# Kernel tuning notes

Measured on AMD Instinct MI355X. Metric: run time of the kernel, lower is better.

## Reference

```python
import jax, jax.numpy as jnp
import numpy as np

DIM = 2048
HQ = 32
HKV = 8
HEAD_DIM = DIM // HQ          # 64
GROUP = HQ // HKV             # 4 q-heads per kv-head
B, S = 2, 2048


def setup_inputs() -> dict:
    key = jax.random.key(0)
    ks = jax.random.split(key, 12)
    sc_in = 1.0 / np.sqrt(DIM)   # lecun_normal fan-in scaling
    inp = {
        "q": jax.random.normal(ks[0], (B, S, DIM), jnp.float32),
        "k": jax.random.normal(ks[1], (B, S, DIM), jnp.float32),
        "v": jax.random.normal(ks[2], (B, S, DIM), jnp.float32),
        # causal 0/1 mask: module computes scores -= 1/mask + 1, so 0 -> -inf (masked), 1 -> -2 (softmax-invariant shift)
        "mask": jnp.tril(jnp.ones((S, S), jnp.int32)),
        "Wq": jax.random.normal(ks[3], (DIM, HQ * HEAD_DIM), jnp.float32) * sc_in,
        "bq": jnp.zeros((HQ * HEAD_DIM,), jnp.float32),
        "Wk": jax.random.normal(ks[4], (DIM, HKV * HEAD_DIM), jnp.float32) * sc_in,
        "bk": jnp.zeros((HKV * HEAD_DIM,), jnp.float32),
        "Wv": jax.random.normal(ks[5], (DIM, HKV * HEAD_DIM), jnp.float32) * sc_in,
        "bv": jnp.zeros((HKV * HEAD_DIM,), jnp.float32),
        "Wo": jax.random.normal(ks[6], (DIM, DIM), jnp.float32) * (1.0 / np.sqrt(DIM)),
        "bo": jnp.zeros((DIM,), jnp.float32),
    }
    return inp


def reference(q, k, v, mask, Wq, bq, Wk, bk, Wv, bv, Wo, bo):
    b, s, _ = q.shape
    # projections -> per-head layout
    qx = (q @ Wq + bq).reshape(b, s, HKV, GROUP, HEAD_DIM)   # grouped q-heads
    kx = (k @ Wk + bk).reshape(b, s, HKV, HEAD_DIM)
    vx = (v @ Wv + bv).reshape(b, s, HKV, HEAD_DIM)
    # scores[b, h, g, i, j] = q_i . k_j ; same math as repeating kv heads GROUP times
    scores = jnp.einsum('bihgd,bjhd->bhgij', qx, kx) / jnp.sqrt(
        jnp.asarray(HEAD_DIM, qx.dtype))
    # module's masking: scores -= 1/mask + 1  (mask==0 -> -inf, mask==1 -> -2)
    scores = scores - (1.0 / mask.astype(scores.dtype) + 1.0)
    probs = jax.nn.softmax(scores, axis=-1)
    out = jnp.einsum('bhgij,bjhd->bihgd', probs, vx).reshape(b, s, DIM)
    out = out @ Wo + bo
    return out
```

## Files before the change

kernel.cpp:

```cpp
#include <hip/hip_runtime.h>

typedef unsigned short u16;
typedef unsigned int u32;
typedef __attribute__((ext_vector_type(8))) short short8v;
typedef __attribute__((ext_vector_type(4))) float f32x4;

#define DIM 2048
#define HQN 32
#define HKVN 8
#define HD 64
#define BB 2
#define SS 2048
#define MTOT (BB*SS)
#define NKV (HKVN*HD)

__device__ __forceinline__ u16 f2bf(float f){
  u32 u = __float_as_uint(f);
  u += 0x7FFFu + ((u >> 16) & 1u);
  return (u16)(u >> 16);
}

__device__ __forceinline__ u32 cvtpk(float a, float b){
  u32 r; asm("v_cvt_pk_bf16_f32 %0, %1, %2" : "=v"(r) : "v"(a), "v"(b)); return r;
}

__device__ __forceinline__ void gload_lds16(const void* g, void* l){
  __builtin_amdgcn_global_load_lds((const __attribute__((address_space(1))) u32*)g,
                                   (__attribute__((address_space(3))) u32*)l, 16, 0, 0);
}

#define WAITVM_(N) asm volatile("s_waitcnt vmcnt(" #N ")" ::: "memory")
#define WAITVM(N) WAITVM_(N)
#define CFENCE()  asm volatile("" ::: "memory")
#define BARF()    do { CFENCE(); __builtin_amdgcn_s_barrier(); CFENCE(); } while(0)
#define MF(a,b,cc) __builtin_amdgcn_mfma_f32_16x16x32_bf16((a),(b),(cc),0,0,0)

__global__ __launch_bounds__(256) void cast3_kernel(const float4* __restrict__ q,
                                                    const float4* __restrict__ k,
                                                    const float4* __restrict__ v,
                                                    u16* __restrict__ qo,
                                                    u16* __restrict__ ko,
                                                    u16* __restrict__ vo, int n4){
  const int z = blockIdx.y;
  const float4* in = z==0 ? q : (z==1 ? k : v);
  u16* out = z==0 ? qo : (z==1 ? ko : vo);
  int i = blockIdx.x*256 + threadIdx.x;
  if (i < n4){
    float4 f = in[i];
    union { u16 s[4]; unsigned long long u; } r;
    r.s[0]=f2bf(f.x); r.s[1]=f2bf(f.y); r.s[2]=f2bf(f.z); r.s[3]=f2bf(f.w);
    *(unsigned long long*)(out + (size_t)i*4) = r.u;
  }
}

__global__ __launch_bounds__(256) void transpose4_kernel(const float* __restrict__ Wq,
                                                         const float* __restrict__ Wk,
                                                         const float* __restrict__ Wv,
                                                         const float* __restrict__ Wo,
                                                         u16* __restrict__ WqT,
                                                         u16* __restrict__ WkT,
                                                         u16* __restrict__ WvT,
                                                         u16* __restrict__ WoT){
  const int z = blockIdx.z;
  const float* W = z==0?Wq:(z==1?Wk:(z==2?Wv:Wo));
  u16* WT = z==0?WqT:(z==1?WkT:(z==2?WvT:WoT));
  const int N = (z==1||z==2) ? NKV : DIM;
  const int K = DIM;
  int n0 = blockIdx.x*32, k0 = blockIdx.y*32;
  if (n0 >= N) return;
  __shared__ float tile[32][33];
  int tx = threadIdx.x & 31, ty = threadIdx.x >> 5;
  #pragma unroll
  for (int i=0;i<4;i++){
    int kk = ty + i*8;
    tile[kk][tx] = W[(size_t)(k0+kk)*N + n0 + tx];
  }
  __syncthreads();
  #pragma unroll
  for (int i=0;i<4;i++){
    int n = ty + i*8;
    WT[(size_t)(n0+n)*K + k0 + tx] = f2bf(tile[tx][n]);
  }
}

__global__ __launch_bounds__(512, 2) void gemm_qkv_kernel(const u16* __restrict__ Aq,
                                                          const u16* __restrict__ Ak,
                                                          const u16* __restrict__ Av,
                                                          const u16* __restrict__ BT,
                                                          const float* __restrict__ bq,
                                                          const float* __restrict__ bk,
                                                          const float* __restrict__ bv,
                                                          u16* __restrict__ Qp,
                                                          u16* __restrict__ Kp,
                                                          u16* __restrict__ Vp){
  __shared__ __align__(16) u16 lds[65536];
  char* ldsb = (char*)lds;
  const int t = threadIdx.x, lane = t & 63, w = t >> 6;
  const int wm = w >> 2, wn = w & 3, g = lane >> 4, c = lane & 15;
  int bid = blockIdx.x;
  bid = (bid & 7)*24 + (bid >> 3);
  const int mt = bid / 12, nt = bid - mt*12;
  const int m0 = mt*256, n0 = nt*256;
  const int seg = (n0 >= 2560) ? 2 : (n0 >= 2048 ? 1 : 0);
  const u16* A = seg==0 ? Aq : (seg==1 ? Ak : Av);
  const float* bias = seg==0 ? bq : (seg==1 ? bk : bv);
  const int nbase = seg==0 ? 0 : (seg==1 ? 2048 : 2560);

  const int rA = t >> 3;
  const int kc = ((t & 7) ^ (rA & 7)) * 8;
  const u16* gA = A  + (size_t)(m0 + rA)*DIM + kc;
  const u16* gB = BT + (size_t)(n0 + ((rA>>5)<<6) + (rA & 31))*DIM + kc;

  const u32 ko0 = (u32)((g*16) ^ ((c&7)<<4));
  const u32 ko1 = (u32)((64 + g*16) ^ ((c&7)<<4));
  const u32 aoff = wm*8192 + c*128;
  const u32 boff = wn*4096 + c*128;

#define STGA_(PA, KT, ABASE) do{ \
    gload_lds16(gA + (size_t)(KT)*64 + (size_t)((PA)*64)*DIM,       ldsb + (ABASE) + (PA)*16384 + t*16); \
    gload_lds16(gA + (size_t)(KT)*64 + (size_t)((PA)*64+128)*DIM,   ldsb + (ABASE) + (PA)*16384 + 8192 + t*16); }while(0)
#define STGB_(PB, KT, BBASE) do{ \
    gload_lds16(gB + (size_t)(KT)*64 + (size_t)((PB)*32)*DIM,       ldsb + (BBASE) + (PB)*16384 + t*16); \
    gload_lds16(gB + (size_t)(KT)*64 + (size_t)((PB)*32+128)*DIM,   ldsb + (BBASE) + (PB)*16384 + 8192 + t*16); }while(0)
#define LD8(OFF) (*(const short8v*)(ldsb + (OFF)))

  const f32x4 fzero = {0.f,0.f,0.f,0.f};
  f32x4 acc[8][4];
  #pragma unroll
  for (int i=0;i<8;i++)
    #pragma unroll
    for (int j=0;j<4;j++) acc[i][j] = fzero;

#define MM16(FM0, FN0) do{ __builtin_amdgcn_s_setprio(1); \
    _Pragma("unroll") for (int q=0;q<4;q++) \
      _Pragma("unroll") for (int s=0;s<2;s++){ \
        acc[(FM0)+q][(FN0)+s] = MF(a_[q][0], b_[s][0], acc[(FM0)+q][(FN0)+s]); \
        acc[(FM0)+q][(FN0)+s] = MF(a_[q][1], b_[s][1], acc[(FM0)+q][(FN0)+s]); } \
    __builtin_amdgcn_s_setprio(0); }while(0)

#define RD_A(PABASE) do{ _Pragma("unroll") for (int q=0;q<4;q++){ \
    a_[q][0] = LD8((PABASE) + aoff + q*2048 + ko0); \
    a_[q][1] = LD8((PABASE) + aoff + q*2048 + ko1); } }while(0)
#define RD_B(PBBASE) do{ _Pragma("unroll") for (int q=0;q<2;q++){ \
    b_[q][0] = LD8((PBBASE) + boff + q*2048 + ko0); \
    b_[q][1] = LD8((PBBASE) + boff + q*2048 + ko1); } }while(0)

#define QSTEP(TT, CUR, DOSTG, TAIL) do{ \
    const u32 AC = (CUR)*32768,  BC = 65536 + (CUR)*32768; \
    const u32 AN = (CUR^1)*32768, BN = 65536 + (CUR^1)*32768; \
    short8v a_[4][2], b_[2][2]; \
    RD_A(AC); RD_B(BC); \
    if (DOSTG) STGA_(0, (TT)+1, AN); \
    BARF(); \
    MM16(0,0); \
    if (TAIL) { WAITVM(2); } else { WAITVM(4); } \
    BARF(); \
    RD_B(BC + 16384); \
    if (DOSTG) STGB_(0, (TT)+1, BN); \
    BARF(); \
    MM16(0,2); \
    if (TAIL) { WAITVM(0); } else { WAITVM(4); } \
    BARF(); \
    RD_A(AC + 16384); \
    if (DOSTG) STGB_(1, (TT)+1, BN); \
    BARF(); \
    MM16(4,2); \
    BARF(); \
    RD_B(BC); \
    if (DOSTG) STGA_(1, (TT)+1, AN); \
    BARF(); \
    MM16(4,0); \
    if (!TAIL) { WAITVM(4); } \
    BARF(); \
  }while(0)

  STGA_(0, 0, 0); STGB_(0, 0, 65536); STGB_(1, 0, 65536); STGA_(1, 0, 0);
  WAITVM(0);
  BARF();

  #pragma unroll 1
  for (int tt = 0; tt < 30; tt += 2){
    QSTEP(tt,   0, 1, 0);
    QSTEP(tt+1, 1, 1, 0);
  }
  QSTEP(30, 0, 1, 0);
  QSTEP(31, 1, 0, 1);
#undef QSTEP

  WAITVM(0);
  __syncthreads();

  u16* st = lds + w*8192;
  if (seg == 2){
    #pragma unroll
    for (int fm=0; fm<8; fm++){
      #pragma unroll
      for (int fn=0; fn<4; fn++){
        float bvv = bias[n0 - nbase + wn*64 + fn*16 + c];
        int vbase = (fm>>1)*2048 + fn*512 + (g*16 + c)*8 + (fm&1)*4;
        *(u32*)&st[vbase]     = cvtpk(acc[fm][fn][0]+bvv, acc[fm][fn][1]+bvv);
        *(u32*)&st[vbase + 2] = cvtpk(acc[fm][fn][2]+bvv, acc[fm][fn][3]+bvv);
      }
    }
  } else {
    #pragma unroll
    for (int fm=0; fm<8; fm++){
      #pragma unroll
      for (int fn=0; fn<4; fn++){
        float bvv = bias[n0 - nbase + wn*64 + fn*16 + c];
        int sbase = (fm>>1)*2048 + ((fm&1)*2 + (fn>>1))*512 + (c>>2)*128 + (fn&1)*4 + (c&3);
        #pragma unroll
        for (int r=0; r<4; r++)
          st[sbase + (4*g + r)*8] = f2bf(acc[fm][fn][r] + bvv);
      }
    }
  }
  __syncthreads();
  {
    const int bb = m0 >> 11;
    const int st0 = ((m0 & 2047) >> 5) + wm*4;
    u16* dst;
    if (seg == 0)      dst = Qp + (((size_t)bb*HQN  + (n0>>6)        + wn) << 17);
    else if (seg == 1) dst = Kp + (((size_t)bb*HKVN + ((n0-2048)>>6) + wn) << 17);
    else               dst = Vp + (((size_t)bb*HKVN + ((n0-2560)>>6) + wn) << 17);
    dst += (size_t)st0*2048;
    #pragma unroll
    for (int i=0;i<16;i++)
      *(short8v*)(dst + lane*8 + i*512) = *(const short8v*)(st + lane*8 + i*512);
  }
#undef STGA_
#undef STGB_
#undef RD_A
#undef RD_B
#undef MM16
}

__global__ __launch_bounds__(512, 2) void gemm_o_kernel(const u16* __restrict__ A,
                                                        const u16* __restrict__ BT,
                                                        const float* __restrict__ bias,
                                                        float* __restrict__ C){
  __shared__ __align__(16) u16 lds[49152];
  char* ldsb = (char*)lds;
  const int t = threadIdx.x, lane = t & 63, w = t >> 6;
  const int wm = w >> 2, wn = w & 3, g = lane >> 4, c = lane & 15;
  int bid = blockIdx.x;
  bid = (bid & 7)*32 + (bid >> 3);
  const int m0 = (bid >> 4)*256, n0 = (bid & 15)*128;

  const int rA = t >> 3;
  const int kc = ((t & 7) ^ (rA & 7)) * 8;
  const u16* gA = A  + (size_t)(m0 + rA)*DIM + kc;
  const u16* gB = BT + (size_t)(n0 + ((rA>>4)<<5) + (rA & 15))*DIM + kc;

  const u32 ko0 = (u32)((g*16) ^ ((c&7)<<4));
  const u32 ko1 = (u32)((64 + g*16) ^ ((c&7)<<4));
  const u32 aoff = wm*8192 + c*128;
  const u32 boffo = wn*2048 + c*128;

#define STGA_(PA, KT, ABASE) do{ \
    gload_lds16(gA + (size_t)(KT)*64 + (size_t)((PA)*64)*DIM,       ldsb + (ABASE) + (PA)*16384 + t*16); \
    gload_lds16(gA + (size_t)(KT)*64 + (size_t)((PA)*64+128)*DIM,   ldsb + (ABASE) + (PA)*16384 + 8192 + t*16); }while(0)
#define STGB_(PB, KT, BBASE) do{ \
    gload_lds16(gB + (size_t)(KT)*64 + (size_t)((PB)*16)*DIM,       ldsb + (BBASE) + (PB)*8192 + t*16); }while(0)
#define LD8(OFF) (*(const short8v*)(ldsb + (OFF)))

  const f32x4 fzero = {0.f,0.f,0.f,0.f};
  f32x4 acc[8][2];
  #pragma unroll
  for (int i=0;i<8;i++){ acc[i][0] = fzero; acc[i][1] = fzero; }

#define MMO(FM0, FN) do{ __builtin_amdgcn_s_setprio(1); \
    _Pragma("unroll") for (int q=0;q<4;q++){ \
      acc[(FM0)+q][FN] = MF(a_[q][0], b_[0], acc[(FM0)+q][FN]); \
      acc[(FM0)+q][FN] = MF(a_[q][1], b_[1], acc[(FM0)+q][FN]); } \
    __builtin_amdgcn_s_setprio(0); }while(0)

#define RD_A(PABASE) do{ _Pragma("unroll") for (int q=0;q<4;q++){ \
    a_[q][0] = LD8((PABASE) + aoff + q*2048 + ko0); \
    a_[q][1] = LD8((PABASE) + aoff + q*2048 + ko1); } }while(0)
#define RD_B(PBBASE) do{ \
    b_[0] = LD8((PBBASE) + boffo + ko0); \
    b_[1] = LD8((PBBASE) + boffo + ko1); }while(0)

#define OSTEP(TT, CUR, DOSTG, TAIL) do{ \
    const u32 AC = (CUR)*32768,  BC = 65536 + (CUR)*16384; \
    const u32 AN = (CUR^1)*32768, BN = 65536 + (CUR^1)*16384; \
    short8v a_[4][2], b_[2]; \
    RD_A(AC); RD_B(BC); \
    if (DOSTG) STGA_(0, (TT)+1, AN); \
    BARF(); \
    MMO(0,0); \
    if (TAIL) { WAITVM(2); } else { WAITVM(4); } \
    BARF(); \
    RD_B(BC + 8192); \
    if (DOSTG) STGB_(0, (TT)+1, BN); \
    BARF(); \
    MMO(0,1); \
    if (TAIL) { WAITVM(0); } else { WAITVM(3); } \
    BARF(); \
    RD_A(AC + 16384); \
    if (DOSTG) STGB_(1, (TT)+1, BN); \
    BARF(); \
    MMO(4,1); \
    BARF(); \
    RD_B(BC); \
    if (DOSTG) STGA_(1, (TT)+1, AN); \
    BARF(); \
    MMO(4,0); \
    if (!TAIL) { WAITVM(3); } \
    BARF(); \
  }while(0)

  STGA_(0, 0, 0); STGB_(0, 0, 65536); STGB_(1, 0, 65536); STGA_(1, 0, 0);
  WAITVM(0);
  BARF();

  #pragma unroll 1
  for (int tt = 0; tt < 30; tt += 2){
    OSTEP(tt,   0, 1, 0);
    OSTEP(tt+1, 1, 1, 0);
  }
  OSTEP(30, 0, 1, 0);
  OSTEP(31, 1, 0, 1);
#undef OSTEP

  #pragma unroll
  for (int fm=0; fm<8; fm++){
    #pragma unroll
    for (int fn=0; fn<2; fn++){
      int n = n0 + wn*32 + fn*16 + c;
      float bvv = bias[n];
      #pragma unroll
      for (int r=0; r<4; r++){
        int m = m0 + wm*128 + fm*16 + 4*g + r;
        C[(size_t)m*DIM + n] = acc[fm][fn][r] + bvv;
      }
    }
  }
#undef STGA_
#undef STGB_
#undef RD_A
#undef RD_B
#undef MMO
}

__global__ __launch_bounds__(256) void attn_kernel(const u16* __restrict__ Qp,
                                                   const u16* __restrict__ Kp,
                                                   const u16* __restrict__ Vp,
                                                   u16* __restrict__ Aout){
  const int grp = blockIdx.x & 15;
  const int jj  = blockIdx.x >> 4;
  const int b   = grp >> 3;
  const int hkv = grp & 7;
  const int t = threadIdx.x;
  const int lane = t & 63, w = t >> 6;
  const int g = lane >> 4, c = lane & 15;
  const int hq = hkv*4 + w;

  __shared__ __align__(16) u16 Kt[2][2048];
  __shared__ __align__(16) u16 Vt[2][2048];

  const u16* Kb = Kp + (((size_t)b*HKVN + hkv) << 17);
  const u16* Vb = Vp + (((size_t)b*HKVN + hkv) << 17);
  const u16* Qb = Qp + (((size_t)b*HQN + hq) << 17);
  const float SCL = 0.18033688011112042f;
  const f32x4 fzero = {0.f,0.f,0.f,0.f};

  for (int half = 0; half < 2; ++half){
    const int T = half ? jj : (63 - jj);

    short8v qf[2][2];
    {
      const u16* qs = Qb + (size_t)T*2048 + lane*8;
      qf[0][0] = *(const short8v*)(qs);
      qf[0][1] = *(const short8v*)(qs + 512);
      qf[1][0] = *(const short8v*)(qs + 1024);
      qf[1][1] = *(const short8v*)(qs + 1536);
    }
    float l_r[2] = {0.f, 0.f};
    f32x4 o[2][4];
    #pragma unroll
    for (int qi=0; qi<2; qi++)
      #pragma unroll
      for (int f=0; f<4; f++) o[qi][f] = fzero;

    gload_lds16(Kb + t*8, &Kt[0][t*8]);
    gload_lds16(Vb + t*8, &Vt[0][t*8]);
    asm volatile("s_waitcnt vmcnt(0)" ::: "memory");
    __syncthreads();

    int cur = 0;
    for (int kt = 0; kt <= T; ++kt){
      if (kt < T){
        gload_lds16(Kb + (size_t)(kt+1)*2048 + t*8, &Kt[cur^1][t*8]);
        gload_lds16(Vb + (size_t)(kt+1)*2048 + t*8, &Vt[cur^1][t*8]);
      }
      short8v kf0 = *(const short8v*)&Kt[cur][lane*8];
      short8v kf1 = *(const short8v*)&Kt[cur][512 + lane*8];
      short8v kf2 = *(const short8v*)&Kt[cur][1024 + lane*8];
      short8v kf3 = *(const short8v*)&Kt[cur][1536 + lane*8];
      short8v vf0 = *(const short8v*)&Vt[cur][lane*8];
      short8v vf1 = *(const short8v*)&Vt[cur][512 + lane*8];
      short8v vf2 = *(const short8v*)&Vt[cur][1024 + lane*8];
      short8v vf3 = *(const short8v*)&Vt[cur][1536 + lane*8];
      const bool diag = (kt == T);
      #pragma unroll
      for (int qi=0; qi<2; qi++){
        f32x4 s0 = fzero, s1 = fzero;
        __builtin_amdgcn_s_setprio(1);
        s0 = MF(kf0, qf[qi][0], s0);
        s0 = MF(kf1, qf[qi][1], s0);
        s1 = MF(kf2, qf[qi][0], s1);
        s1 = MF(kf3, qf[qi][1], s1);
        __builtin_amdgcn_s_setprio(0);
        float p0[4], p1[4];
        #pragma unroll
        for (int r=0; r<4; r++){
          p0[r] = __builtin_amdgcn_exp2f(s0[r]*SCL);
          p1[r] = __builtin_amdgcn_exp2f(s1[r]*SCL);
        }
        if (diag){
          const int qloc = qi*16 + c;
          #pragma unroll
          for (int r=0; r<4; r++){
            if (4*g + r      > qloc) p0[r] = 0.f;
            if (16 + 4*g + r > qloc) p1[r] = 0.f;
          }
        }
        l_r[qi] += (p0[0]+p0[1]) + (p0[2]+p0[3]) + (p1[0]+p1[1]) + (p1[2]+p1[3]);
        union { u32 u[4]; short8v v; } pu;
        pu.u[0] = cvtpk(p0[0], p0[1]);
        pu.u[1] = cvtpk(p0[2], p0[3]);
        pu.u[2] = cvtpk(p1[0], p1[1]);
        pu.u[3] = cvtpk(p1[2], p1[3]);
        __builtin_amdgcn_s_setprio(1);
        o[qi][0] = MF(pu.v, vf0, o[qi][0]);
        o[qi][1] = MF(pu.v, vf1, o[qi][1]);
        o[qi][2] = MF(pu.v, vf2, o[qi][2]);
        o[qi][3] = MF(pu.v, vf3, o[qi][3]);
        __builtin_amdgcn_s_setprio(0);
      }
      asm volatile("s_waitcnt vmcnt(0)" ::: "memory");
      __syncthreads();
      cur ^= 1;
    }

    #pragma unroll
    for (int qi=0; qi<2; qi++){
      float ls = l_r[qi];
      ls += __shfl_xor(ls, 16);
      ls += __shfl_xor(ls, 32);
      float li = 1.0f / ls;
      float lf[4];
      #pragma unroll
      for (int r=0; r<4; r++) lf[r] = __shfl(li, 4*g + r);
      #pragma unroll
      for (int f=0; f<4; f++){
        #pragma unroll
        for (int r=0; r<4; r++){
          int q = T*32 + qi*16 + 4*g + r;
          Aout[((size_t)b*SS + q)*DIM + hq*HD + f*16 + c] = f2bf(o[qi][f][r]*lf[r]);
        }
      }
    }
  }
}

extern "C" void kernel_launch(void* const* d_in, const int* in_sizes, int n_in,
                              void* d_out, int out_size, void* d_ws, size_t ws_size,
                              hipStream_t stream){
  const float* q  = (const float*)d_in[0];
  const float* k  = (const float*)d_in[1];
  const float* v  = (const float*)d_in[2];
  const float* Wq = (const float*)d_in[4];
  const float* bq = (const float*)d_in[5];
  const float* Wk = (const float*)d_in[6];
  const float* bk = (const float*)d_in[7];
  const float* Wv = (const float*)d_in[8];
  const float* bv = (const float*)d_in[9];
  const float* Wo = (const float*)d_in[10];
  const float* bo = (const float*)d_in[11];
  float* out = (float*)d_out;

  char* ws = (char*)d_ws;
  u16* q_bf = (u16*)ws; ws += (size_t)MTOT*DIM*2;
  u16* k_bf = (u16*)ws; ws += (size_t)MTOT*DIM*2;
  u16* v_bf = (u16*)ws; ws += (size_t)MTOT*DIM*2;
  u16* WqT  = (u16*)ws; ws += (size_t)DIM*DIM*2;
  u16* WkT  = (u16*)ws; ws += (size_t)NKV*DIM*2;
  u16* WvT  = (u16*)ws; ws += (size_t)NKV*DIM*2;
  u16* WoT  = (u16*)ws; ws += (size_t)DIM*DIM*2;
  u16* Qp   = (u16*)ws; ws += (size_t)MTOT*DIM*2;
  u16* Kp   = (u16*)ws; ws += (size_t)MTOT*NKV*2;
  u16* Vp   = (u16*)ws; ws += (size_t)MTOT*NKV*2;
  u16* attn = (u16*)ws; ws += (size_t)MTOT*DIM*2;

  const int n4 = MTOT*DIM/4;
  cast3_kernel<<<dim3(n4/256, 3), 256, 0, stream>>>((const float4*)q, (const float4*)k,
                                                    (const float4*)v, q_bf, k_bf, v_bf, n4);
  transpose4_kernel<<<dim3(DIM/32, DIM/32, 4), 256, 0, stream>>>(Wq, Wk, Wv, Wo,
                                                                 WqT, WkT, WvT, WoT);
  gemm_qkv_kernel<<<192, 512, 0, stream>>>(q_bf, k_bf, v_bf, WqT,
                                           bq, bk, bv, Qp, Kp, Vp);
  attn_kernel<<<512, 256, 0, stream>>>(Qp, Kp, Vp, attn);
  gemm_o_kernel<<<256, 512, 0, stream>>>(attn, WoT, bo, out);
}
```

Measured before the change: 198.8 us.

## Cut barriers in GEMM steps, widen O-GEMM B tile, use 4-slot KV ring

The QKV GEMM step now keeps both B fragment sets in registers, which removes several barriers per K-step and the reload of B. The output GEMM switches to a 64-wide B tile per wave with two MFMA columns, halving the number of phases and barriers. The attention kernel replaces its double-buffered K/V tiles with a 4-slot LDS ring prefetched three tiles ahead, using partial vmcnt waits instead of a full drain each iteration. Both GEMMs drop to one block per CU in their launch bounds, trading occupancy for more registers.

```diff
diff --git a/kernel.cpp b/kernel.cpp
--- a/kernel.cpp
+++ b/kernel.cpp
@@ -31,8 +31,7 @@
 
 #define WAITVM_(N) asm volatile("s_waitcnt vmcnt(" #N ")" ::: "memory")
 #define WAITVM(N) WAITVM_(N)
-#define CFENCE()  asm volatile("" ::: "memory")
-#define BARF()    do { CFENCE(); __builtin_amdgcn_s_barrier(); CFENCE(); } while(0)
+#define BARF()    do { asm volatile("" ::: "memory"); __builtin_amdgcn_s_barrier(); asm volatile("" ::: "memory"); } while(0)
 #define MF(a,b,cc) __builtin_amdgcn_mfma_f32_16x16x32_bf16((a),(b),(cc),0,0,0)
 
 __global__ __launch_bounds__(256) void cast3_kernel(const float4* __restrict__ q,
@@ -83,7 +82,7 @@
   }
 }
 
-__global__ __launch_bounds__(512, 2) void gemm_qkv_kernel(const u16* __restrict__ Aq,
+__global__ __launch_bounds__(512, 1) void gemm_qkv_kernel(const u16* __restrict__ Aq,
                                                           const u16* __restrict__ Ak,
                                                           const u16* __restrict__ Av,
                                                           const u16* __restrict__ BT,
@@ -131,51 +130,50 @@
     #pragma unroll
     for (int j=0;j<4;j++) acc[i][j] = fzero;
 
-#define MM16(FM0, FN0) do{ __builtin_amdgcn_s_setprio(1); \
-    _Pragma("unroll") for (int q=0;q<4;q++) \
-      _Pragma("unroll") for (int s=0;s<2;s++){ \
-        acc[(FM0)+q][(FN0)+s] = MF(a_[q][0], b_[s][0], acc[(FM0)+q][(FN0)+s]); \
-        acc[(FM0)+q][(FN0)+s] = MF(a_[q][1], b_[s][1], acc[(FM0)+q][(FN0)+s]); } \
-    __builtin_amdgcn_s_setprio(0); }while(0)
-
 #define RD_A(PABASE) do{ _Pragma("unroll") for (int q=0;q<4;q++){ \
     a_[q][0] = LD8((PABASE) + aoff + q*2048 + ko0); \
     a_[q][1] = LD8((PABASE) + aoff + q*2048 + ko1); } }while(0)
-#define RD_B(PBBASE) do{ _Pragma("unroll") for (int q=0;q<2;q++){ \
-    b_[q][0] = LD8((PBBASE) + boff + q*2048 + ko0); \
-    b_[q][1] = LD8((PBBASE) + boff + q*2048 + ko1); } }while(0)
+#define RD_B(DST, PBBASE) do{ _Pragma("unroll") for (int s=0;s<2;s++){ \
+    DST[s][0] = LD8((PBBASE) + boff + s*2048 + ko0); \
+    DST[s][1] = LD8((PBBASE) + boff + s*2048 + ko1); } }while(0)
+
+#define MM16(BSRC, FM0, FN0) do{ __builtin_amdgcn_s_setprio(1); \
+    _Pragma("unroll") for (int q=0;q<4;q++) \
+      _Pragma("unroll") for (int s=0;s<2;s++){ \
+        acc[(FM0)+q][(FN0)+s] = MF(a_[q][0], BSRC[s][0], acc[(FM0)+q][(FN0)+s]); \
+        acc[(FM0)+q][(FN0)+s] = MF(a_[q][1], BSRC[s][1], acc[(FM0)+q][(FN0)+s]); } \
+    __builtin_amdgcn_s_setprio(0); }while(0)
 
 #define QSTEP(TT, CUR, DOSTG, TAIL) do{ \
-    const u32 AC = (CUR)*32768,  BC = 65536 + (CUR)*32768; \
-    const u32 AN = (CUR^1)*32768, BN = 65536 + (CUR^1)*32768; \
-    short8v a_[4][2], b_[2][2]; \
-    RD_A(AC); RD_B(BC); \
+    const u32 AC = (CUR)*32768,  BC2 = 65536 + (CUR)*32768; \
+    const u32 AN = (CUR^1)*32768, BN2 = 65536 + (CUR^1)*32768; \
+    short8v a_[4][2], b0_[2][2], b1_[2][2]; \
+     \
+    RD_A(AC); RD_B(b0_, BC2); \
     if (DOSTG) STGA_(0, (TT)+1, AN); \
-    BARF(); \
-    MM16(0,0); \
+    MM16(b0_, 0, 0); \
     if (TAIL) { WAITVM(2); } else { WAITVM(4); } \
     BARF(); \
-    RD_B(BC + 16384); \
-    if (DOSTG) STGB_(0, (TT)+1, BN); \
-    BARF(); \
-    MM16(0,2); \
+     \
+    RD_B(b1_, BC2 + 16384); \
+    if (DOSTG) STGB_(0, (TT)+1, BN2); \
+    MM16(b1_, 0, 2); \
     if (TAIL) { WAITVM(0); } else { WAITVM(4); } \
     BARF(); \
+     \
     RD_A(AC + 16384); \
-    if (DOSTG) STGB_(1, (TT)+1, BN); \
+    if (DOSTG) STGB_(1, (TT)+1, BN2); \
+    MM16(b1_, 4, 2); \
     BARF(); \
-    MM16(4,2); \
-    BARF(); \
-    RD_B(BC); \
+     \
     if (DOSTG) STGA_(1, (TT)+1, AN); \
-    BARF(); \
-    MM16(4,0); \
+    MM16(b0_, 4, 0); \
     if (!TAIL) { WAITVM(4); } \
     BARF(); \
   }while(0)
 
   STGA_(0, 0, 0); STGB_(0, 0, 65536); STGB_(1, 0, 65536); STGA_(1, 0, 0);
-  WAITVM(0);
+  WAITVM(4);
   BARF();
 
   #pragma unroll 1
@@ -235,7 +233,7 @@
 #undef MM16
 }
 
-__global__ __launch_bounds__(512, 2) void gemm_o_kernel(const u16* __restrict__ A,
+__global__ __launch_bounds__(512, 1) void gemm_o_kernel(const u16* __restrict__ A,
                                                         const u16* __restrict__ BT,
                                                         const float* __restrict__ bias,
                                                         float* __restrict__ C){
@@ -250,18 +248,19 @@
   const int rA = t >> 3;
   const int kc = ((t & 7) ^ (rA & 7)) * 8;
   const u16* gA = A  + (size_t)(m0 + rA)*DIM + kc;
-  const u16* gB = BT + (size_t)(n0 + ((rA>>4)<<5) + (rA & 15))*DIM + kc;
+  const u16* gB = BT + (size_t)(n0 + rA)*DIM + kc;
 
   const u32 ko0 = (u32)((g*16) ^ ((c&7)<<4));
   const u32 ko1 = (u32)((64 + g*16) ^ ((c&7)<<4));
   const u32 aoff = wm*8192 + c*128;
-  const u32 boffo = wn*2048 + c*128;
+  const u32 boffo = wn*4096 + c*128;
 
 #define STGA_(PA, KT, ABASE) do{ \
     gload_lds16(gA + (size_t)(KT)*64 + (size_t)((PA)*64)*DIM,       ldsb + (ABASE) + (PA)*16384 + t*16); \
     gload_lds16(gA + (size_t)(KT)*64 + (size_t)((PA)*64+128)*DIM,   ldsb + (ABASE) + (PA)*16384 + 8192 + t*16); }while(0)
-#define STGB_(PB, KT, BBASE) do{ \
-    gload_lds16(gB + (size_t)(KT)*64 + (size_t)((PB)*16)*DIM,       ldsb + (BBASE) + (PB)*8192 + t*16); }while(0)
+#define STGB_O(KT, BBASE) do{ \
+    gload_lds16(gB + (size_t)(KT)*64,                     ldsb + (BBASE) + t*16); \
+    gload_lds16(gB + (size_t)(KT)*64 + (size_t)64*DIM,    ldsb + (BBASE) + 8192 + t*16); }while(0)
 #define LD8(OFF) (*(const short8v*)(ldsb + (OFF)))
 
   const f32x4 fzero = {0.f,0.f,0.f,0.f};
@@ -269,50 +268,40 @@
   #pragma unroll
   for (int i=0;i<8;i++){ acc[i][0] = fzero; acc[i][1] = fzero; }
 
-#define MMO(FM0, FN) do{ __builtin_amdgcn_s_setprio(1); \
-    _Pragma("unroll") for (int q=0;q<4;q++){ \
-      acc[(FM0)+q][FN] = MF(a_[q][0], b_[0], acc[(FM0)+q][FN]); \
-      acc[(FM0)+q][FN] = MF(a_[q][1], b_[1], acc[(FM0)+q][FN]); } \
-    __builtin_amdgcn_s_setprio(0); }while(0)
-
 #define RD_A(PABASE) do{ _Pragma("unroll") for (int q=0;q<4;q++){ \
     a_[q][0] = LD8((PABASE) + aoff + q*2048 + ko0); \
     a_[q][1] = LD8((PABASE) + aoff + q*2048 + ko1); } }while(0)
-#define RD_B(PBBASE) do{ \
-    b_[0] = LD8((PBBASE) + boffo + ko0); \
-    b_[1] = LD8((PBBASE) + boffo + ko1); }while(0)
+#define RD_BO(BBASE) do{ _Pragma("unroll") for (int s=0;s<2;s++){ \
+    b_[s][0] = LD8((BBASE) + boffo + s*2048 + ko0); \
+    b_[s][1] = LD8((BBASE) + boffo + s*2048 + ko1); } }while(0)
+
+#define MMO(FM0) do{ __builtin_amdgcn_s_setprio(1); \
+    _Pragma("unroll") for (int q=0;q<4;q++) \
+      _Pragma("unroll") for (int s=0;s<2;s++){ \
+        acc[(FM0)+q][s] = MF(a_[q][0], b_[s][0], acc[(FM0)+q][s]); \
+        acc[(FM0)+q][s] = MF(a_[q][1], b_[s][1], acc[(FM0)+q][s]); } \
+    __builtin_amdgcn_s_setprio(0); }while(0)
 
 #define OSTEP(TT, CUR, DOSTG, TAIL) do{ \
-    const u32 AC = (CUR)*32768,  BC = 65536 + (CUR)*16384; \
-    const u32 AN = (CUR^1)*32768, BN = 65536 + (CUR^1)*16384; \
-    short8v a_[4][2], b_[2]; \
-    RD_A(AC); RD_B(BC); \
-    if (DOSTG) STGA_(0, (TT)+1, AN); \
+    const u32 AC = (CUR)*32768,  BC2 = 65536 + (CUR)*16384; \
+    const u32 AN = (CUR^1)*32768, BN2 = 65536 + (CUR^1)*16384; \
+    short8v a_[4][2], b_[2][2]; \
+     \
+    RD_A(AC); RD_BO(BC2); \
+    if (DOSTG) { STGA_(0, (TT)+1, AN); STGB_O((TT)+1, BN2); } \
+    MMO(0); \
+    if (TAIL) { WAITVM(0); } else { WAITVM(4); } \
     BARF(); \
-    MMO(0,0); \
-    if (TAIL) { WAITVM(2); } else { WAITVM(4); } \
-    BARF(); \
-    RD_B(BC + 8192); \
-    if (DOSTG) STGB_(0, (TT)+1, BN); \
-    BARF(); \
-    MMO(0,1); \
-    if (TAIL) { WAITVM(0); } else { WAITVM(3); } \
-    BARF(); \
+     \
     RD_A(AC + 16384); \
-    if (DOSTG) STGB_(1, (TT)+1, BN); \
-    BARF(); \
-    MMO(4,1); \
-    BARF(); \
-    RD_B(BC); \
     if (DOSTG) STGA_(1, (TT)+1, AN); \
-    BARF(); \
-    MMO(4,0); \
-    if (!TAIL) { WAITVM(3); } \
+    MMO(4); \
+    if (!TAIL) { WAITVM(2); } \
     BARF(); \
   }while(0)
 
-  STGA_(0, 0, 0); STGB_(0, 0, 65536); STGB_(1, 0, 65536); STGA_(1, 0, 0);
-  WAITVM(0);
+  STGA_(0, 0, 0); STGB_O(0, 65536); STGA_(1, 0, 0);
+  WAITVM(2);
   BARF();
 
   #pragma unroll 1
@@ -327,20 +316,20 @@
   #pragma unroll
   for (int fm=0; fm<8; fm++){
     #pragma unroll
-    for (int fn=0; fn<2; fn++){
-      int n = n0 + wn*32 + fn*16 + c;
+    for (int s=0; s<2; s++){
+      int n = n0 + wn*32 + s*16 + c;
       float bvv = bias[n];
       #pragma unroll
       for (int r=0; r<4; r++){
         int m = m0 + wm*128 + fm*16 + 4*g + r;
-        C[(size_t)m*DIM + n] = acc[fm][fn][r] + bvv;
+        C[(size_t)m*DIM + n] = acc[fm][s][r] + bvv;
       }
     }
   }
 #undef STGA_
-#undef STGB_
+#undef STGB_O
 #undef RD_A
-#undef RD_B
+#undef RD_BO
 #undef MMO
 }
 
@@ -357,8 +346,7 @@
   const int g = lane >> 4, c = lane & 15;
   const int hq = hkv*4 + w;
 
-  __shared__ __align__(16) u16 Kt[2][2048];
-  __shared__ __align__(16) u16 Vt[2][2048];
+  __shared__ __align__(16) u16 ring[4][2][2048];
 
   const u16* Kb = Kp + (((size_t)b*HKVN + hkv) << 17);
   const u16* Vb = Vp + (((size_t)b*HKVN + hkv) << 17);
@@ -368,6 +356,8 @@
 
   for (int half = 0; half < 2; ++half){
     const int T = half ? jj : (63 - jj);
+
+    BARF();
 
     short8v qf[2][2];
     {
@@ -384,25 +374,31 @@
       #pragma unroll
       for (int f=0; f<4; f++) o[qi][f] = fzero;
 
-    gload_lds16(Kb + t*8, &Kt[0][t*8]);
-    gload_lds16(Vb + t*8, &Vt[0][t*8]);
-    asm volatile("s_waitcnt vmcnt(0)" ::: "memory");
-    __syncthreads();
-
-    int cur = 0;
+    #pragma unroll
+    for (int s=0; s<3; s++){
+      const int tc = s > T ? T : s;
+      gload_lds16(Kb + (size_t)tc*2048 + t*8, &ring[s][0][t*8]);
+      gload_lds16(Vb + (size_t)tc*2048 + t*8, &ring[s][1][t*8]);
+    }
+
     for (int kt = 0; kt <= T; ++kt){
-      if (kt < T){
-        gload_lds16(Kb + (size_t)(kt+1)*2048 + t*8, &Kt[cur^1][t*8]);
-        gload_lds16(Vb + (size_t)(kt+1)*2048 + t*8, &Vt[cur^1][t*8]);
+      WAITVM(4);
+      BARF();
+      const int sl = kt & 3;
+      short8v kf0 = *(const short8v*)&ring[sl][0][lane*8];
+      short8v kf1 = *(const short8v*)&ring[sl][0][512 + lane*8];
+      short8v kf2 = *(const short8v*)&ring[sl][0][1024 + lane*8];
+      short8v kf3 = *(const short8v*)&ring[sl][0][1536 + lane*8];
+      short8v vf0 = *(const short8v*)&ring[sl][1][lane*8];
+      short8v vf1 = *(const short8v*)&ring[sl][1][512 + lane*8];
+      short8v vf2 = *(const short8v*)&ring[sl][1][1024 + lane*8];
+      short8v vf3 = *(const short8v*)&ring[sl][1][1536 + lane*8];
+      {
+        const int tc = (kt+3) > T ? T : (kt+3);
+        const int sn = (kt+3) & 3;
+        gload_lds16(Kb + (size_t)tc*2048 + t*8, &ring[sn][0][t*8]);
+        gload_lds16(Vb + (size_t)tc*2048 + t*8, &ring[sn][1][t*8]);
       }
-      short8v kf0 = *(const short8v*)&Kt[cur][lane*8];
-      short8v kf1 = *(const short8v*)&Kt[cur][512 + lane*8];
-      short8v kf2 = *(const short8v*)&Kt[cur][1024 + lane*8];
-      short8v kf3 = *(const short8v*)&Kt[cur][1536 + lane*8];
-      short8v vf0 = *(const short8v*)&Vt[cur][lane*8];
-      short8v vf1 = *(const short8v*)&Vt[cur][512 + lane*8];
-      short8v vf2 = *(const short8v*)&Vt[cur][1024 + lane*8];
-      short8v vf3 = *(const short8v*)&Vt[cur][1536 + lane*8];
       const bool diag = (kt == T);
       #pragma unroll
       for (int qi=0; qi<2; qi++){
@@ -440,9 +436,6 @@
         o[qi][3] = MF(pu.v, vf3, o[qi][3]);
         __builtin_amdgcn_s_setprio(0);
       }
-      asm volatile("s_waitcnt vmcnt(0)" ::: "memory");
-      __syncthreads();
-      cur ^= 1;
     }
 
     #pragma unroll
```

After: 196.5 us. No clear change (-1.2%).
